# Performance work log

Measured on AMD Instinct MI355X. Metric: run time of the kernel, lower is better.

## Reference

```python
import jax, jax.numpy as jnp
import numpy as np

DIM_IN_Q = 4096
DIM_IN_K = 4096
MSG_DIM = 4096


def setup_inputs() -> dict:
    key = jax.random.key(0)
    ks = jax.random.split(key, 8)
    s_q = 1.0 / np.sqrt(DIM_IN_Q)
    s_l = 1.0 / np.sqrt(MSG_DIM)
    s_k = 1.0 / np.sqrt(DIM_IN_K)
    return {
        # forward args (2-D path; N == msg_dim and M == 6 are structural requirements)
        "data_q": jax.random.normal(ks[0], (MSG_DIM, DIM_IN_Q), jnp.float32),
        "data_k": jax.random.normal(ks[1], (6, DIM_IN_K), jnp.float32),
        # learned parameters (torch nn.Linear layout: [out, in])
        "W_q": jax.random.uniform(ks[2], (MSG_DIM, DIM_IN_Q), jnp.float32, -s_q, s_q),
        "b_q": jax.random.uniform(ks[3], (MSG_DIM,), jnp.float32, -s_q, s_q),
        "W_lin": jax.random.uniform(ks[4], (6, MSG_DIM), jnp.float32, -s_l, s_l),
        "b_lin": jax.random.uniform(ks[5], (6,), jnp.float32, -s_l, s_l),
        "W_k": jax.random.uniform(ks[6], (MSG_DIM, DIM_IN_K), jnp.float32, -s_k, s_k),
        "b_k": jax.random.uniform(ks[7], (MSG_DIM,), jnp.float32, -s_k, s_k),
    }


def _relu6(x):
    return jnp.clip(x, 0.0, 6.0)


def reference(data_q, data_k, W_q, b_q, W_lin, b_lin, W_k, b_k):
    # q: [N=msg_dim, msg_dim]
    q = data_q @ W_q.T + b_q
    # secondary projection over transposed q: [msg_dim, N] -> [msg_dim, 6]
    new_q = q.T @ W_lin.T + b_lin
    # k: [6, msg_dim]
    k = data_k @ W_k.T + b_k
    context = new_q.T  # [6, msg_dim]
    # custom modulation: relu6(k^2 + 2k + context*(1+|k|))
    k_mod = _relu6(jnp.square(k) + 2.0 * k + context * (1.0 + jnp.abs(k)))
    # dot: [msg_dim, 6], scaled by sqrt(msg_dim)
    dot = q @ k_mod.T
    return dot / np.sqrt(MSG_DIM).astype(np.float32)
```

## Files before the change

### kernel.cpp

```cpp
#include <hip/hip_runtime.h>
#include <hip/hip_bf16.h>
#include <stdint.h>

#define NDIM 4096

typedef __attribute__((ext_vector_type(8))) __bf16 bf16x8;
typedef __attribute__((ext_vector_type(4))) float f32x4;

__device__ inline void g2lds16(const void* g, void* l) {
  __builtin_amdgcn_global_load_lds(
      (const __attribute__((address_space(1))) void*)g,
      (__attribute__((address_space(3))) void*)l, 16, 0, 0);
}

__device__ inline unsigned short f2bf(float f) {
  union { float f; uint32_t u; } c; c.f = f;
  uint32_t u = c.u;
  uint32_t r = ((u >> 16) & 1u) + 0x7FFFu;
  return (unsigned short)((u + r) >> 16);
}

__global__ __launch_bounds__(256) void convert_kernel(const float* __restrict__ in,
                                                      ushort* __restrict__ out) {
  int idx = blockIdx.x * 256 + threadIdx.x;
  float4 v = ((const float4*)in)[idx];
  ushort4 o;
  o.x = f2bf(v.x); o.y = f2bf(v.y); o.z = f2bf(v.z); o.w = f2bf(v.w);
  ((ushort4*)out)[idx] = o;
}

#define BM 128
#define BN 128
#define BK 64

__global__ __launch_bounds__(256) void gemm_q_kernel(const ushort* __restrict__ Abf,
                                                     const ushort* __restrict__ Bbf,
                                                     const float* __restrict__ bias,
                                                     float* __restrict__ q) {
  __shared__ __align__(16) ushort As[BM * BK];
  __shared__ __align__(16) ushort Bs[BN * BK];

  const int tid = threadIdx.x;
  int wg = blockIdx.x;
  int cpx = gridDim.x >> 3;
  int swz = (wg & 7) * cpx + (wg >> 3);
  const int bi = swz >> 5;
  const int bj = swz & 31;
  const int i0 = bi * BM, j0 = bj * BN;

  const int lane = tid & 63;
  const int wave = tid >> 6;
  const int wr = wave >> 1, wc = wave & 1;
  const int l15 = lane & 15, lg = lane >> 4;

  const int srow = tid >> 3;
  const int scol = (tid & 7) * 8;

  f32x4 acc[4][4] = {};

  for (int k0 = 0; k0 < NDIM; k0 += BK) {
    __syncthreads();
#pragma unroll
    for (int p = 0; p < 4; ++p) {
      const int r = p * 32 + srow;
      g2lds16(Abf + (size_t)(i0 + r) * NDIM + k0 + scol, &As[r * BK + scol]);
      g2lds16(Bbf + (size_t)(j0 + r) * NDIM + k0 + scol, &Bs[r * BK + scol]);
    }
    asm volatile("s_waitcnt vmcnt(0)" ::: "memory");
    __syncthreads();

#pragma unroll
    for (int kk = 0; kk < BK / 32; ++kk) {
      bf16x8 af[4], bfr[4];
#pragma unroll
      for (int m = 0; m < 4; ++m)
        af[m] = *(const bf16x8*)&As[(wr * 64 + m * 16 + l15) * BK + kk * 32 + lg * 8];
#pragma unroll
      for (int n = 0; n < 4; ++n)
        bfr[n] = *(const bf16x8*)&Bs[(wc * 64 + n * 16 + l15) * BK + kk * 32 + lg * 8];
#pragma unroll
      for (int m = 0; m < 4; ++m)
#pragma unroll
        for (int n = 0; n < 4; ++n)
          acc[m][n] = __builtin_amdgcn_mfma_f32_16x16x32_bf16(af[m], bfr[n], acc[m][n], 0, 0, 0);
    }
  }

#pragma unroll
  for (int m = 0; m < 4; ++m) {
    const int row = i0 + wr * 64 + m * 16 + lg * 4;
#pragma unroll
    for (int n = 0; n < 4; ++n) {
      const int col = j0 + wc * 64 + n * 16 + l15;
      const float bv = bias[col];
#pragma unroll
      for (int r = 0; r < 4; ++r)
        q[(size_t)(row + r) * NDIM + col] = acc[m][n][r] + bv;
    }
  }
}

__global__ __launch_bounds__(256) void gemv_k_kernel(const float* __restrict__ data_k,
                                                     const float* __restrict__ W_k,
                                                     const float* __restrict__ b_k,
                                                     float* __restrict__ k_out) {
  const int wave = threadIdx.x >> 6, lane = threadIdx.x & 63;
  const int m = blockIdx.x * 4 + wave;
  const float4* W = (const float4*)(W_k + (size_t)m * NDIM);
  const float4* D = (const float4*)data_k;
  float acc[6] = {0.f, 0.f, 0.f, 0.f, 0.f, 0.f};
  for (int it = lane; it < NDIM / 4; it += 64) {
    float4 w = W[it];
#pragma unroll
    for (int j = 0; j < 6; ++j) {
      float4 d = D[j * (NDIM / 4) + it];
      acc[j] += w.x * d.x + w.y * d.y + w.z * d.z + w.w * d.w;
    }
  }
#pragma unroll
  for (int j = 0; j < 6; ++j)
#pragma unroll
    for (int off = 1; off < 64; off <<= 1) acc[j] += __shfl_xor(acc[j], off);
  if (lane == 0) {
    const float bv = b_k[m];
#pragma unroll
    for (int j = 0; j < 6; ++j) k_out[j * NDIM + m] = acc[j] + bv;
  }
}

__global__ __launch_bounds__(256) void newq_kernel(const float* __restrict__ q,
                                                   const float* __restrict__ W_lin,
                                                   float* __restrict__ newq_t) {
  const int m = blockIdx.x * 256 + threadIdx.x;
  const int n0 = blockIdx.y * 128;
  float acc[6] = {0.f, 0.f, 0.f, 0.f, 0.f, 0.f};
  for (int n = n0; n < n0 + 128; ++n) {
    const float qv = q[(size_t)n * NDIM + m];
#pragma unroll
    for (int j = 0; j < 6; ++j) acc[j] += qv * W_lin[j * NDIM + n];
  }
#pragma unroll
  for (int j = 0; j < 6; ++j) atomicAdd(&newq_t[j * NDIM + m], acc[j]);
}

__global__ __launch_bounds__(256) void kmod_kernel(const float* __restrict__ k_in,
                                                   const float* __restrict__ newq_t,
                                                   const float* __restrict__ b_lin,
                                                   float* __restrict__ k_mod) {
  const int idx = blockIdx.x * 256 + threadIdx.x;
  const int j = idx >> 12;
  const float kv = k_in[idx];
  const float ctx = newq_t[idx] + b_lin[j];
  float v = kv * kv + 2.f * kv + ctx * (1.f + fabsf(kv));
  v = fminf(fmaxf(v, 0.f), 6.f);
  k_mod[idx] = v;
}

__global__ __launch_bounds__(256) void dot_kernel(const float* __restrict__ q,
                                                  const float* __restrict__ k_mod,
                                                  float* __restrict__ out) {
  const int wave = threadIdx.x >> 6, lane = threadIdx.x & 63;
  const int n = blockIdx.x * 4 + wave;
  const float4* Q = (const float4*)(q + (size_t)n * NDIM);
  const float4* KM = (const float4*)k_mod;
  float acc[6] = {0.f, 0.f, 0.f, 0.f, 0.f, 0.f};
  for (int it = lane; it < NDIM / 4; it += 64) {
    float4 qv = Q[it];
#pragma unroll
    for (int j = 0; j < 6; ++j) {
      float4 km = KM[j * (NDIM / 4) + it];
      acc[j] += qv.x * km.x + qv.y * km.y + qv.z * km.z + qv.w * km.w;
    }
  }
#pragma unroll
  for (int j = 0; j < 6; ++j)
#pragma unroll
    for (int off = 1; off < 64; off <<= 1) acc[j] += __shfl_xor(acc[j], off);
  if (lane == 0) {
#pragma unroll
    for (int j = 0; j < 6; ++j) out[n * 6 + j] = acc[j] * 0.015625f;
  }
}

extern "C" void kernel_launch(void* const* d_in, const int* in_sizes, int n_in,
                              void* d_out, int out_size, void* d_ws, size_t ws_size,
                              hipStream_t stream) {
  const float* data_q = (const float*)d_in[0];
  const float* data_k = (const float*)d_in[1];
  const float* W_q    = (const float*)d_in[2];
  const float* b_q    = (const float*)d_in[3];
  const float* W_lin  = (const float*)d_in[4];
  const float* b_lin  = (const float*)d_in[5];
  const float* W_k    = (const float*)d_in[6];
  const float* b_k    = (const float*)d_in[7];
  float* out = (float*)d_out;

  char* ws = (char*)d_ws;
  ushort* Abf   = (ushort*)ws;
  ushort* Bbf   = (ushort*)(ws + ((size_t)32 << 20));
  float*  q     = (float*)(ws + ((size_t)64 << 20));
  float*  k_arr = (float*)(ws + ((size_t)128 << 20));
  float*  newq  = k_arr + 6 * NDIM;
  float*  kmod  = newq + 6 * NDIM;

  hipMemsetAsync(newq, 0, 6 * NDIM * sizeof(float), stream);

  convert_kernel<<<16384, 256, 0, stream>>>(data_q, Abf);
  convert_kernel<<<16384, 256, 0, stream>>>(W_q, Bbf);
  gemm_q_kernel<<<1024, 256, 0, stream>>>(Abf, Bbf, b_q, q);
  gemv_k_kernel<<<1024, 256, 0, stream>>>(data_k, W_k, b_k, k_arr);
  newq_kernel<<<dim3(16, 32), 256, 0, stream>>>(q, W_lin, newq);
  kmod_kernel<<<96, 256, 0, stream>>>(k_arr, newq, b_lin, kmod);
  dot_kernel<<<1024, 256, 0, stream>>>(q, kmod, out);
}
```

Measured before the change: 450.5 us.

## Double-buffer 256x256 GEMM with swizzled LDS and store q as bf16

Rewrites the q GEMM to use 256x256 tiles with 512 threads, double-buffered LDS loads prefetched two k-steps ahead, XOR-swizzled LDS addressing to avoid bank conflicts, and priority hints around the MFMA bursts. The q output is written as bf16 instead of fp32, which halves the write traffic and the reads in the newq and dot kernels. In exchange, q is rounded to bf16 before the secondary projection and the final dot, which adds precision loss. The kernel also needs much more LDS per block.

```diff
diff --git a/kernel.cpp b/kernel.cpp
--- a/kernel.cpp
+++ b/kernel.cpp
@@ -18,6 +18,11 @@
   uint32_t u = c.u;
   uint32_t r = ((u >> 16) & 1u) + 0x7FFFu;
   return (unsigned short)((u + r) >> 16);
+}
+
+__device__ inline float bf2f(ushort u) {
+  union { uint32_t u; float f; } c; c.u = ((uint32_t)u) << 16;
+  return c.f;
 }
 
 __global__ __launch_bounds__(256) void convert_kernel(const float* __restrict__ in,
@@ -29,75 +34,124 @@
   ((ushort4*)out)[idx] = o;
 }
 
-#define BM 128
-#define BN 128
-#define BK 64
-
-__global__ __launch_bounds__(256) void gemm_q_kernel(const ushort* __restrict__ Abf,
-                                                     const ushort* __restrict__ Bbf,
-                                                     const float* __restrict__ bias,
-                                                     float* __restrict__ q) {
-  __shared__ __align__(16) ushort As[BM * BK];
-  __shared__ __align__(16) ushort Bs[BN * BK];
+
+__device__ inline bf16x8 ldfrag(const ushort* buf, int row, int kk, int lg) {
+  int idx = (row * 64 + kk * 32 + lg * 8) ^ ((row & 7) << 3);
+  return *(const bf16x8*)&buf[idx];
+}
+
+__global__ __launch_bounds__(512, 2) void gemm_q_kernel(const ushort* __restrict__ Abf,
+                                                        const ushort* __restrict__ Bbf,
+                                                        const float* __restrict__ bias,
+                                                        ushort* __restrict__ qout) {
+  __shared__ __align__(16) ushort As[2][16384];
+  __shared__ __align__(16) ushort Bs[2][16384];
 
   const int tid = threadIdx.x;
-  int wg = blockIdx.x;
-  int cpx = gridDim.x >> 3;
-  int swz = (wg & 7) * cpx + (wg >> 3);
-  const int bi = swz >> 5;
-  const int bj = swz & 31;
-  const int i0 = bi * BM, j0 = bj * BN;
-
-  const int lane = tid & 63;
-  const int wave = tid >> 6;
-  const int wr = wave >> 1, wc = wave & 1;
+  const int wg = blockIdx.x;
+  const int swz = (wg & 7) * 32 + (wg >> 3);
+  const int i0 = (swz >> 4) * 256;
+  const int j0 = (swz & 15) * 256;
+
+  const int lane = tid & 63, wid = tid >> 6;
+  const int wr = wid >> 2, wc = wid & 3;
   const int l15 = lane & 15, lg = lane >> 4;
 
   const int srow = tid >> 3;
-  const int scol = (tid & 7) * 8;
-
-  f32x4 acc[4][4] = {};
-
-  for (int k0 = 0; k0 < NDIM; k0 += BK) {
-    __syncthreads();
-#pragma unroll
-    for (int p = 0; p < 4; ++p) {
-      const int r = p * 32 + srow;
-      g2lds16(Abf + (size_t)(i0 + r) * NDIM + k0 + scol, &As[r * BK + scol]);
-      g2lds16(Bbf + (size_t)(j0 + r) * NDIM + k0 + scol, &Bs[r * BK + scol]);
-    }
-    asm volatile("s_waitcnt vmcnt(0)" ::: "memory");
-    __syncthreads();
-
-#pragma unroll
-    for (int kk = 0; kk < BK / 32; ++kk) {
-      bf16x8 af[4], bfr[4];
+  const int scol = ((tid & 7) ^ (srow & 7)) * 8;
+
+#define STAGE(tensor, r0, k0v, buf)                                          \
+  {                                                                          \
+    _Pragma("unroll")                                                        \
+    for (int i_ = 0; i_ < 4; ++i_) {                                         \
+      g2lds16(tensor + (size_t)((r0) + i_ * 64 + srow) * NDIM + (k0v) + scol,\
+              (void*)&buf[i_ * 4096 + tid * 8]);                             \
+    }                                                                        \
+  }
+
+  f32x4 acc[8][4] = {};
+
+  STAGE(Abf, i0, 0, As[0]);
+  STAGE(Bbf, j0, 0, Bs[0]);
+  STAGE(Abf, i0, 64, As[1]);
+  STAGE(Bbf, j0, 64, Bs[1]);
+  asm volatile("s_waitcnt vmcnt(8)" ::: "memory");
+  __builtin_amdgcn_sched_barrier(0);
+  __builtin_amdgcn_s_barrier();
+  __builtin_amdgcn_sched_barrier(0);
+
+  for (int kt = 0; kt < 64; ++kt) {
+    const int cur = kt & 1;
+    const ushort* A = As[cur];
+    const ushort* B = Bs[cur];
+
+    bf16x8 a0[4][2], a1[4][2], bfr[4][2];
+#pragma unroll
+    for (int m = 0; m < 4; ++m)
+#pragma unroll
+      for (int kk = 0; kk < 2; ++kk)
+        a0[m][kk] = ldfrag(A, wr * 128 + m * 16 + l15, kk, lg);
+#pragma unroll
+    for (int n = 0; n < 4; ++n)
+#pragma unroll
+      for (int kk = 0; kk < 2; ++kk)
+        bfr[n][kk] = ldfrag(B, wc * 64 + n * 16 + l15, kk, lg);
+#pragma unroll
+    for (int m = 0; m < 4; ++m)
+#pragma unroll
+      for (int kk = 0; kk < 2; ++kk)
+        a1[m][kk] = ldfrag(A, wr * 128 + 64 + m * 16 + l15, kk, lg);
+
+    __builtin_amdgcn_s_setprio(1);
+#pragma unroll
+    for (int kk = 0; kk < 2; ++kk)
 #pragma unroll
       for (int m = 0; m < 4; ++m)
-        af[m] = *(const bf16x8*)&As[(wr * 64 + m * 16 + l15) * BK + kk * 32 + lg * 8];
-#pragma unroll
-      for (int n = 0; n < 4; ++n)
-        bfr[n] = *(const bf16x8*)&Bs[(wc * 64 + n * 16 + l15) * BK + kk * 32 + lg * 8];
+#pragma unroll
+        for (int n = 0; n < 4; ++n)
+          acc[m][n] = __builtin_amdgcn_mfma_f32_16x16x32_bf16(a0[m][kk], bfr[n][kk], acc[m][n], 0, 0, 0);
+    __builtin_amdgcn_s_setprio(0);
+
+    asm volatile("s_waitcnt lgkmcnt(0)" ::: "memory");
+    __builtin_amdgcn_sched_barrier(0);
+    __builtin_amdgcn_s_barrier();
+    __builtin_amdgcn_sched_barrier(0);
+
+    const int knext = ((kt + 2) & 63) * 64;
+    STAGE(Abf, i0, knext, As[cur]);
+    STAGE(Bbf, j0, knext, Bs[cur]);
+
+    __builtin_amdgcn_s_setprio(1);
+#pragma unroll
+    for (int kk = 0; kk < 2; ++kk)
 #pragma unroll
       for (int m = 0; m < 4; ++m)
 #pragma unroll
         for (int n = 0; n < 4; ++n)
-          acc[m][n] = __builtin_amdgcn_mfma_f32_16x16x32_bf16(af[m], bfr[n], acc[m][n], 0, 0, 0);
-    }
-  }
-
-#pragma unroll
-  for (int m = 0; m < 4; ++m) {
-    const int row = i0 + wr * 64 + m * 16 + lg * 4;
+          acc[m + 4][n] = __builtin_amdgcn_mfma_f32_16x16x32_bf16(a1[m][kk], bfr[n][kk], acc[m + 4][n], 0, 0, 0);
+    __builtin_amdgcn_s_setprio(0);
+
+    asm volatile("s_waitcnt vmcnt(8)" ::: "memory");
+    __builtin_amdgcn_sched_barrier(0);
+    __builtin_amdgcn_s_barrier();
+    __builtin_amdgcn_sched_barrier(0);
+  }
+
+  float bv[4];
+#pragma unroll
+  for (int n = 0; n < 4; ++n) bv[n] = bias[j0 + wc * 64 + n * 16 + l15];
+#pragma unroll
+  for (int m = 0; m < 8; ++m) {
+    const int row = i0 + wr * 128 + m * 16 + lg * 4;
 #pragma unroll
     for (int n = 0; n < 4; ++n) {
       const int col = j0 + wc * 64 + n * 16 + l15;
-      const float bv = bias[col];
 #pragma unroll
       for (int r = 0; r < 4; ++r)
-        q[(size_t)(row + r) * NDIM + col] = acc[m][n][r] + bv;
+        qout[(size_t)(row + r) * NDIM + col] = f2bf(acc[m][n][r] + bv[n]);
     }
   }
+#undef STAGE
 }
 
 __global__ __launch_bounds__(256) void gemv_k_kernel(const float* __restrict__ data_k,
@@ -128,14 +182,14 @@
   }
 }
 
-__global__ __launch_bounds__(256) void newq_kernel(const float* __restrict__ q,
+__global__ __launch_bounds__(256) void newq_kernel(const ushort* __restrict__ q,
                                                    const float* __restrict__ W_lin,
                                                    float* __restrict__ newq_t) {
   const int m = blockIdx.x * 256 + threadIdx.x;
   const int n0 = blockIdx.y * 128;
   float acc[6] = {0.f, 0.f, 0.f, 0.f, 0.f, 0.f};
   for (int n = n0; n < n0 + 128; ++n) {
-    const float qv = q[(size_t)n * NDIM + m];
+    const float qv = bf2f(q[(size_t)n * NDIM + m]);
 #pragma unroll
     for (int j = 0; j < 6; ++j) acc[j] += qv * W_lin[j * NDIM + n];
   }
@@ -156,20 +210,30 @@
   k_mod[idx] = v;
 }
 
-__global__ __launch_bounds__(256) void dot_kernel(const float* __restrict__ q,
+__global__ __launch_bounds__(256) void dot_kernel(const ushort* __restrict__ q,
                                                   const float* __restrict__ k_mod,
                                                   float* __restrict__ out) {
   const int wave = threadIdx.x >> 6, lane = threadIdx.x & 63;
   const int n = blockIdx.x * 4 + wave;
-  const float4* Q = (const float4*)(q + (size_t)n * NDIM);
-  const float4* KM = (const float4*)k_mod;
+  const uint4* Q = (const uint4*)(q + (size_t)n * NDIM);
   float acc[6] = {0.f, 0.f, 0.f, 0.f, 0.f, 0.f};
-  for (int it = lane; it < NDIM / 4; it += 64) {
-    float4 qv = Q[it];
+  for (int it = lane; it < 512; it += 64) {
+    uint4 v = Q[it];
+    float qf[8];
+    qf[0] = __builtin_bit_cast(float, v.x << 16);
+    qf[1] = __builtin_bit_cast(float, v.x & 0xffff0000u);
+    qf[2] = __builtin_bit_cast(float, v.y << 16);
+    qf[3] = __builtin_bit_cast(float, v.y & 0xffff0000u);
+    qf[4] = __builtin_bit_cast(float, v.z << 16);
+    qf[5] = __builtin_bit_cast(float, v.z & 0xffff0000u);
+    qf[6] = __builtin_bit_cast(float, v.w << 16);
+    qf[7] = __builtin_bit_cast(float, v.w & 0xffff0000u);
 #pragma unroll
     for (int j = 0; j < 6; ++j) {
-      float4 km = KM[j * (NDIM / 4) + it];
-      acc[j] += qv.x * km.x + qv.y * km.y + qv.z * km.z + qv.w * km.w;
+      const float4* KM = (const float4*)(k_mod + j * NDIM);
+      float4 k0 = KM[it * 2], k1 = KM[it * 2 + 1];
+      acc[j] += qf[0] * k0.x + qf[1] * k0.y + qf[2] * k0.z + qf[3] * k0.w
+              + qf[4] * k1.x + qf[5] * k1.y + qf[6] * k1.z + qf[7] * k1.w;
     }
   }
 #pragma unroll
@@ -198,8 +262,8 @@
   char* ws = (char*)d_ws;
   ushort* Abf   = (ushort*)ws;
   ushort* Bbf   = (ushort*)(ws + ((size_t)32 << 20));
-  float*  q     = (float*)(ws + ((size_t)64 << 20));
-  float*  k_arr = (float*)(ws + ((size_t)128 << 20));
+  ushort* q_bf  = (ushort*)(ws + ((size_t)64 << 20));
+  float*  k_arr = (float*)(ws + ((size_t)96 << 20));
   float*  newq  = k_arr + 6 * NDIM;
   float*  kmod  = newq + 6 * NDIM;
 
@@ -207,9 +271,9 @@
 
   convert_kernel<<<16384, 256, 0, stream>>>(data_q, Abf);
   convert_kernel<<<16384, 256, 0, stream>>>(W_q, Bbf);
-  gemm_q_kernel<<<1024, 256, 0, stream>>>(Abf, Bbf, b_q, q);
+  gemm_q_kernel<<<256, 512, 0, stream>>>(Abf, Bbf, b_q, q_bf);
   gemv_k_kernel<<<1024, 256, 0, stream>>>(data_k, W_k, b_k, k_arr);
-  newq_kernel<<<dim3(16, 32), 256, 0, stream>>>(q, W_lin, newq);
+  newq_kernel<<<dim3(16, 32), 256, 0, stream>>>(q_bf, W_lin, newq);
   kmod_kernel<<<96, 256, 0, stream>>>(k_arr, newq, b_lin, kmod);
-  dot_kernel<<<1024, 256, 0, stream>>>(q, kmod, out);
-}
+  dot_kernel<<<1024, 256, 0, stream>>>(q_bf, kmod, out);
+}
```

Result: no change. 450.6 us (+0.0%).
